# Performance work log

Hardware: AMD Instinct MI355X
Metric: run time of the kernel (lower is better)

Reference implementation:

```python
import jax, jax.numpy as jnp
import numpy as np

B, C, W, H = 8192, 512, 14, 4
D = C // H  # head dim = 128


def setup_inputs() -> dict:
    key = jax.random.key(0)
    ks = jax.random.split(key, 8)
    s = 1.0 / np.sqrt(C).astype(np.float32)
    return {
        "x": jax.random.normal(ks[0], (B, C, W), jnp.float32),
        "Wq": jax.random.normal(ks[1], (C, C), jnp.float32) * s,
        "bq": jax.random.normal(ks[2], (C,), jnp.float32) * 0.01,
        "Wk": jax.random.normal(ks[3], (C, C), jnp.float32) * s,
        "bk": jax.random.normal(ks[4], (C,), jnp.float32) * 0.01,
        "Wv": jax.random.normal(ks[5], (C, C), jnp.float32) * s,
        "bv": jax.random.normal(ks[6], (C,), jnp.float32) * 0.01,
        "rel_w": jax.random.normal(ks[7], (1, H, D, W), jnp.float32),
    }


def reference(x, Wq, bq, Wk, bk, Wv, bv, rel_w):
    # Conv1d(kernel_size=1) == channel-wise linear: out[b,o,w] = sum_c Wm[o,c]*x[b,c,w] + bm[o]
    def proj(Wm, bm):
        y = jnp.einsum('oc,bcw->bow', Wm, x) + bm[None, :, None]
        return y.reshape(B, H, D, W)

    q = proj(Wq, bq)  # [B,H,D,W]
    k = proj(Wk, bk)
    v = proj(Wv, bv)

    # content-content: q^T k over head dim -> [B,H,W,W]
    cc = jnp.einsum('bhdi,bhdj->bhij', q, k)
    # content-position: rel_w^T q -> [B,H,W,W] (rows = relative position, cols = query pos)
    cp = jnp.einsum('hdi,bhdj->bhij', rel_w[0], q)

    attn = jax.nn.softmax(cc + cp, axis=-1)  # softmax over last dim, as in the original

    # out = v @ attn^T : out[b,h,d,i] = sum_j v[b,h,d,j] * attn[b,h,i,j]
    out = jnp.einsum('bhdj,bhij->bhdi', v, attn)
    return out.reshape(B, C, W)
```

## Files before the change

### kernel.cpp

```cpp
#include <hip/hip_runtime.h>
#include <hip/hip_bf16.h>

typedef __bf16 bf16x8 __attribute__((ext_vector_type(8)));
typedef float f32x4 __attribute__((ext_vector_type(4)));
typedef int i32x4 __attribute__((ext_vector_type(4)));

typedef __attribute__((address_space(1))) const void GVoid;
typedef __attribute__((address_space(3))) void LVoid;

#define SX1 16.0f
#define SX1I 0.0625f
#define SX2 4000.0f
#define SW1 400.0f
#define SW1I 0.0025f
#define SW2 100000.0f
#define SR1 32.0f
#define SR1I 0.03125f
#define SR2 8000.0f
#define SC_QK 1.5625e-4f
#define SC_CP 1.953125e-3f
#define CORR 0.004f
#define QKS 4096.0f
#define QKSI 2.44140625e-4f
#define QKSI2 5.9604644775390625e-8f
#define CPS 256.0f
#define CPSI 3.90625e-3f

static __device__ __forceinline__ float b2f(unsigned short u) {
    union { float f; unsigned int i; } x; x.i = ((unsigned int)u) << 16; return x.f;
}
static __device__ __forceinline__ unsigned short f2b(float f) {
    union { float f; unsigned int u; } x; x.f = f;
    unsigned int r = x.u + 0x7FFFu + ((x.u >> 16) & 1u);
    return (unsigned short)(r >> 16);
}
static __device__ __forceinline__ int q8v(float v, float s) {
    int i = __float2int_rn(v * s);
    return (i > 127) ? 127 : (i < -127 ? -127 : i);
}
static __device__ __forceinline__ short f2s(float v, float s) {
    int i = __float2int_rn(v * s);
    i = (i > 32767) ? 32767 : (i < -32767 ? -32767 : i);
    return (short)i;
}
static __device__ __forceinline__ float s2f(unsigned int pair, int hi, float sc) {
    short s = hi ? (short)(pair >> 16) : (short)(pair & 0xffffu);
    return (float)s * sc;
}
static __device__ __forceinline__ void cvt8(uint4 r, float* o) {
    o[0] = (float)(short)(r.x & 0xffffu); o[1] = (float)(short)(r.x >> 16);
    o[2] = (float)(short)(r.y & 0xffffu); o[3] = (float)(short)(r.y >> 16);
    o[4] = (float)(short)(r.z & 0xffffu); o[5] = (float)(short)(r.z >> 16);
    o[6] = (float)(short)(r.w & 0xffffu); o[7] = (float)(short)(r.w >> 16);
}

__global__ __launch_bounds__(256) void k_prep(const float* __restrict__ Wq, const float* __restrict__ Wk,
                                              const float* __restrict__ Wv, const float* __restrict__ bq,
                                              const float* __restrict__ bk, const float* __restrict__ bv,
                                              const float* __restrict__ relw, char* __restrict__ Wi8,
                                              float* __restrict__ biasA) {
    int o = blockIdx.x;
    int tid = threadIdx.x;
    if (o < 1024) {
        const float* src = (o < 512) ? (Wq + (long)o * 512) : (Wk + (long)(o - 512) * 512);
        char* row = Wi8 + (long)o * 1024;
        for (int c = tid; c < 512; c += 256) {
            float w = src[c];
            int wh = q8v(w, SW1);
            float res = w - (float)wh * SW1I;
            int wl = q8v(res, SW2);
            row[c] = (char)wh;
            row[512 + c] = (char)wl;
        }
    } else if (o < 1536) {
        const float* src = Wv + (long)(o - 1024) * 512;
        char* row = Wi8 + (long)(1152 + (o - 1024)) * 1024;
        for (int c = tid; c < 512; c += 256) {
            float w = src[c];
            int wh = q8v(w, SW1);
            float res = w - (float)wh * SW1I;
            int wl = q8v(res, SW2);
            row[c] = (char)wh;
            row[512 + c] = (char)wl;
        }
    } else if (o < 1592) {
        int t = o - 1536, h = t / 14, i = t - h * 14;
        char* row = Wi8 + (long)(1024 + t) * 1024;
#pragma unroll
        for (int cc = 0; cc < 2; ++cc) {
            int c = tid + cc * 256;
            float acc = 0.f;
            for (int d = 0; d < 128; ++d)
                acc += relw[h * 1792 + d * 14 + i] * Wq[(long)(h * 128 + d) * 512 + c];
            int rh = q8v(acc, SR1);
            float res = acc - (float)rh * SR1I;
            int rl = q8v(res, SR2);
            row[c] = (char)rh;
            row[512 + c] = (char)rl;
        }
        if (tid == 0) {
            float acc = 0.f;
            for (int d = 0; d < 128; ++d) acc += relw[h * 1792 + d * 14 + i] * bq[h * 128 + d];
            biasA[1024 + t] = acc;
        }
    } else {
        for (int i = tid; i < 1664; i += 256) {
            if (i >= 1024 && i < 1080) continue;
            biasA[i] = (i < 512) ? bq[i] : (i < 1024) ? bk[i - 512] : (i < 1152) ? 0.f : bv[i - 1152];
        }
        int* z = (int*)(Wi8 + (long)1080 * 1024);
        for (int idx = tid; idx < 72 * 256; idx += 256) z[idx] = 0;
    }
}

__global__ __launch_bounds__(256) void k_transpose(const float* __restrict__ x,
                                                   char* __restrict__ Ai8, int b0) {
    __shared__ float xl[512 * 15];
    const float* xb = x + (long)(b0 + blockIdx.x) * 7168;
    const float4* xb4 = (const float4*)xb;
    int tid = threadIdx.x;
#pragma unroll
    for (int it = 0; it < 7; ++it) {
        int f = tid + it * 256;
        float4 v = xb4[f];
        float vals[4] = {v.x, v.y, v.z, v.w};
        int e = f * 4;
#pragma unroll
        for (int j = 0; j < 4; ++j) {
            int ee = e + j;
            int c = (ee * 9363) >> 17;
            int w = ee - c * 14;
            xl[c * 15 + w] = vals[j];
        }
    }
    __syncthreads();
    char* irow = Ai8 + (long)blockIdx.x * 14336;
#pragma unroll
    for (int it = 0; it < 7; ++it) {
        int p = tid + it * 256;
        int w = p >> 7, c0 = (p & 127) * 4;
        unsigned int hp = 0, lp = 0;
#pragma unroll
        for (int j = 0; j < 4; ++j) {
            float v = xl[(c0 + j) * 15 + w];
            int xh = q8v(v, SX1);
            float res = v - (float)xh * SX1I;
            int xlo = q8v(res, SX2);
            hp |= ((unsigned int)(xh & 255)) << (8 * j);
            lp |= ((unsigned int)(xlo & 255)) << (8 * j);
        }
        *(unsigned int*)(irow + (long)w * 1024 + c0) = hp;
        *(unsigned int*)(irow + (long)w * 1024 + 512 + c0) = lp;
    }
}

__global__ __launch_bounds__(256, 2) void k_gemmA(const char* __restrict__ Ai8,
                                                  const char* __restrict__ Wi8,
                                                  const float* __restrict__ biasA,
                                                  short* __restrict__ qkI,
                                                  unsigned short* __restrict__ vb, int Mtiles) {
    __shared__ __align__(16) char Ls[2][4][128 * 64];
    int nwg = Mtiles * 13;
    int p = blockIdx.x;
    int xcd = p & 7, o8 = p >> 3;
    int q8_ = nwg >> 3, r8 = nwg & 7;
    int t = (xcd < r8 ? xcd * (q8_ + 1) : r8 * (q8_ + 1) + (xcd - r8) * q8_) + o8;
    int mt = t / 13, nt = t - mt * 13;
    long m0 = (long)mt * 128;
    int n0 = nt * 128;
    bool isv = (nt >= 9);
    int tid = threadIdx.x, lane = tid & 63, wv = tid >> 6;
    int wr = wv >> 1, wc = wv & 1;

    i32x4 accM[4][4], accC[4][4];
#pragma unroll
    for (int i = 0; i < 4; ++i)
#pragma unroll
        for (int j = 0; j < 4; ++j) { accM[i][j] = (i32x4){0, 0, 0, 0}; accC[i][j] = (i32x4){0, 0, 0, 0}; }

#define STAGE(KT, BUF)                                                                           \
    {                                                                                            \
        int kof = (KT) * 64;                                                                     \
        _Pragma("unroll") for (int i = 0; i < 2; ++i) {                                          \
            int row = i * 64 + (tid >> 2);                                                       \
            int gu = (((tid & 3) + (row >> 1)) & 3) << 4;                                        \
            long ao = ((m0 + row) << 10) + kof + gu;                                             \
            long bo = ((long)(n0 + row) << 10) + kof + gu;                                       \
            int dof = i * 4096 + tid * 16;                                                       \
            __builtin_amdgcn_global_load_lds((GVoid*)(Ai8 + ao), (LVoid*)(&Ls[BUF][0][0] + dof), 16, 0, 0); \
            __builtin_amdgcn_global_load_lds((GVoid*)(Ai8 + ao + 512), (LVoid*)(&Ls[BUF][1][0] + dof), 16, 0, 0); \
            __builtin_amdgcn_global_load_lds((GVoid*)(Wi8 + bo), (LVoid*)(&Ls[BUF][2][0] + dof), 16, 0, 0); \
            __builtin_amdgcn_global_load_lds((GVoid*)(Wi8 + bo + 512), (LVoid*)(&Ls[BUF][3][0] + dof), 16, 0, 0); \
        }                                                                                        \
    }

    STAGE(0, 0);
    STAGE(1, 1);
    asm volatile("s_waitcnt vmcnt(8)" ::: "memory");
    __builtin_amdgcn_s_barrier();

    int cur = 0;
    for (int kt = 0; kt < 8; ++kt) {
        const char* Ah = &Ls[cur][0][0];
        const char* Al = &Ls[cur][1][0];
        const char* Bh = &Ls[cur][2][0];
        const char* Bl = &Ls[cur][3][0];
        int U = lane >> 4;
        i32x4 ah[4], al[4], bh[4], bl[4];
#pragma unroll
        for (int mf = 0; mf < 4; ++mf) {
            int row = wr * 64 + mf * 16 + (lane & 15);
            int off = row * 64 + (((U - (row >> 1)) & 3) << 4);
            ah[mf] = *(const i32x4*)(Ah + off);
            al[mf] = *(const i32x4*)(Al + off);
        }
#pragma unroll
        for (int nf = 0; nf < 4; ++nf) {
            int row = wc * 64 + nf * 16 + (lane & 15);
            int off = row * 64 + (((U - (row >> 1)) & 3) << 4);
            bh[nf] = *(const i32x4*)(Bh + off);
            bl[nf] = *(const i32x4*)(Bl + off);
        }
        asm volatile("s_waitcnt lgkmcnt(0)" ::: "memory");
        __builtin_amdgcn_sched_barrier(0);
        __builtin_amdgcn_s_barrier();
        if (kt + 2 < 8) STAGE(kt + 2, cur);

        __builtin_amdgcn_s_setprio(1);
#pragma unroll
        for (int mf = 0; mf < 4; ++mf)
#pragma unroll
            for (int nf = 0; nf < 4; ++nf)
                accM[mf][nf] = __builtin_amdgcn_mfma_i32_16x16x64_i8(ah[mf], bh[nf], accM[mf][nf], 0, 0, 0);
#pragma unroll
        for (int mf = 0; mf < 4; ++mf)
#pragma unroll
            for (int nf = 0; nf < 4; ++nf) {
                accC[mf][nf] = __builtin_amdgcn_mfma_i32_16x16x64_i8(al[mf], bh[nf], accC[mf][nf], 0, 0, 0);
                accC[mf][nf] = __builtin_amdgcn_mfma_i32_16x16x64_i8(ah[mf], bl[nf], accC[mf][nf], 0, 0, 0);
            }
        __builtin_amdgcn_s_setprio(0);

        if (kt < 6) asm volatile("s_waitcnt vmcnt(8)" ::: "memory");
        else        asm volatile("s_waitcnt vmcnt(0)" ::: "memory");
        __builtin_amdgcn_sched_barrier(0);
        __builtin_amdgcn_s_barrier();
        cur ^= 1;
    }
#undef STAGE

    unsigned short* eb = (unsigned short*)&Ls[0][0][0];
#pragma unroll
    for (int nf = 0; nf < 4; ++nf) {
        int ncol = wc * 64 + nf * 16 + (lane & 15);
        int n = n0 + ncol;
        float scale = (n < 1024) ? SC_QK : (n < 1152 ? SC_CP : SC_QK);
        float qsc = (n < 1024) ? QKS : CPS;
        float bb = biasA[n];
#pragma unroll
        for (int mf = 0; mf < 4; ++mf) {
            int rl0 = wr * 64 + mf * 16 + ((lane >> 4) << 2);
#pragma unroll
            for (int r = 0; r < 4; ++r) {
                float val = ((float)accM[mf][nf][r] + CORR * (float)accC[mf][nf][r]) * scale + bb;
                unsigned short sv = isv ? f2b(val) : (unsigned short)f2s(val, qsc);
                int row = rl0 + r;
                eb[row * 128 + ((((ncol >> 3) ^ (row & 7)) << 3) | (ncol & 7))] = sv;
            }
        }
    }
    __syncthreads();
    {
        int row = tid >> 1, half = tid & 1;
        long rb = isv ? ((m0 + row) * 1024 + (long)(n0 - 1152) * 2)
                      : ((m0 + row) * 2304 + (long)n0 * 2);
        char* dst = (isv ? (char*)vb : (char*)qkI) + rb + half * 128;
        const char* src = (const char*)eb + row * 256;
#pragma unroll
        for (int j = 0; j < 8; ++j) {
            int u = half * 8 + j;
            int up = u ^ (row & 7);
            *(uint4*)(dst + j * 16) = *(const uint4*)(src + up * 16);
        }
    }
}

__global__ __launch_bounds__(512) void k_attn(const short* __restrict__ qkI,
                                              const unsigned short* __restrict__ vb,
                                              float* __restrict__ out, int b0) {
    __shared__ unsigned short qsI[14 * 512];
    __shared__ unsigned short ksI[14 * 512];
    __shared__ float sl[56 * 16];
    int tid = threadIdx.x;
    long mb = (long)blockIdx.x * 14;
    const uint4* qk16 = (const uint4*)qkI;
#pragma unroll
    for (int it = 0; it < 4; ++it) {
        int idx = tid + it * 512;
        if (idx < 1792) {
            int w = idx >> 7, c8 = idx & 127;
            uint4 raw = qk16[(mb + w) * 144 + c8];
            int u = c8 & 63;
            unsigned short* base = (c8 < 64) ? qsI : ksI;
            *(uint4*)&base[w * 512 + ((u ^ (w & 7)) << 3)] = raw;
        }
    }
    __syncthreads();
    if (tid < 196) {
        int h = tid / 49, r = tid - h * 49;
        int i0 = (r / 7) * 2, j0 = (r - (r / 7) * 7) * 2;
        float a00 = 0.f, a01 = 0.f, a10 = 0.f, a11 = 0.f;
#pragma unroll
        for (int d8 = 0; d8 < 16; ++d8) {
            int uu = h * 16 + d8;
            uint4 ra = *(const uint4*)&qsI[i0 * 512 + ((uu ^ (i0 & 7)) << 3)];
            uint4 rb = *(const uint4*)&qsI[(i0 + 1) * 512 + ((uu ^ ((i0 + 1) & 7)) << 3)];
            uint4 rc = *(const uint4*)&ksI[j0 * 512 + ((uu ^ (j0 & 7)) << 3)];
            uint4 rd = *(const uint4*)&ksI[(j0 + 1) * 512 + ((uu ^ ((j0 + 1) & 7)) << 3)];
            float qa[8], qb[8], ka[8], kb[8];
            cvt8(ra, qa); cvt8(rb, qb); cvt8(rc, ka); cvt8(rd, kb);
#pragma unroll
            for (int e = 0; e < 8; ++e) {
                a00 += qa[e] * ka[e];
                a01 += qa[e] * kb[e];
                a10 += qb[e] * ka[e];
                a11 += qb[e] * kb[e];
            }
        }
        unsigned int cpa = *(const unsigned int*)&qkI[(mb + j0) * 1152 + 1024 + h * 14 + i0];
        unsigned int cpb = *(const unsigned int*)&qkI[(mb + j0 + 1) * 1152 + 1024 + h * 14 + i0];
        int base = (h * 14 + i0) * 16 + j0;
        sl[base]      = a00 * QKSI2 + s2f(cpa, 0, CPSI);
        sl[base + 16] = a10 * QKSI2 + s2f(cpa, 1, CPSI);
        sl[base + 1]  = a01 * QKSI2 + s2f(cpb, 0, CPSI);
        sl[base + 17] = a11 * QKSI2 + s2f(cpb, 1, CPSI);
    }
    __syncthreads();
    if (tid < 56) {
        float* row = &sl[tid * 16];
        float m = row[0];
#pragma unroll
        for (int j = 1; j < 14; ++j) m = fmaxf(m, row[j]);
        float ex[14]; float sum = 0.f;
#pragma unroll
        for (int j = 0; j < 14; ++j) { ex[j] = __expf(row[j] - m); sum += ex[j]; }
        float inv = 1.f / sum;
#pragma unroll
        for (int j = 0; j < 14; ++j) row[j] = ex[j] * inv;
    }
    __syncthreads();
    int c = tid, h = c >> 7;
    float vr[14];
#pragma unroll
    for (int j = 0; j < 14; ++j) vr[j] = b2f(vb[(mb + j) * 512 + c]);
    float* orow = out + (((long)(b0 + blockIdx.x) * 512 + c) * 14);
    float ob[14];
#pragma unroll
    for (int i = 0; i < 14; ++i) {
        const float* ar = &sl[(h * 14 + i) * 16];
        float a = 0.f;
#pragma unroll
        for (int j = 0; j < 14; ++j) a += vr[j] * ar[j];
        ob[i] = a;
    }
#pragma unroll
    for (int t2 = 0; t2 < 7; ++t2)
        *(float2*)(orow + t2 * 2) = make_float2(ob[2 * t2], ob[2 * t2 + 1]);
}

extern "C" void kernel_launch(void* const* d_in, const int* in_sizes, int n_in,
                              void* d_out, int out_size, void* d_ws, size_t ws_size,
                              hipStream_t stream) {
    const float* x    = (const float*)d_in[0];
    const float* Wq   = (const float*)d_in[1];
    const float* bq   = (const float*)d_in[2];
    const float* Wk   = (const float*)d_in[3];
    const float* bk   = (const float*)d_in[4];
    const float* Wv   = (const float*)d_in[5];
    const float* bv   = (const float*)d_in[6];
    const float* relw = (const float*)d_in[7];
    float* out = (float*)d_out;
    char* ws = (char*)d_ws;

    char*  Wi8   = ws;
    float* biasA = (float*)(ws + 1703936);
    const long WS_DATA = 1712128;

    long avail = (long)ws_size - WS_DATA;
    long nbmax = avail / 60928;
    long NBc = (nbmax / 128) * 128;
    if (NBc > 2048) NBc = 2048;
    if (NBc < 128) NBc = 128;

    char*           Ai8 = ws + WS_DATA;
    short*          qkI = (short*)(Ai8 + NBc * 14336);
    unsigned short* vbw = (unsigned short*)(qkI + NBc * 16128);

    k_prep<<<1593, 256, 0, stream>>>(Wq, Wk, Wv, bq, bk, bv, relw, Wi8, biasA);

    for (int b0 = 0; b0 < 8192; b0 += (int)NBc) {
        int nb = 8192 - b0; if (nb > NBc) nb = (int)NBc;
        int Mtiles = (nb * 14) / 128;
        k_transpose<<<nb, 256, 0, stream>>>(x, Ai8, b0);
        k_gemmA<<<Mtiles * 13, 256, 0, stream>>>(Ai8, Wi8, biasA, qkI, vbw, Mtiles);
        k_attn<<<nb, 512, 0, stream>>>(qkI, vbw, out, b0);
    }
}
```

Before: 636.7 us.

## Load GEMM operands directly from global memory into registers, dropping LDS staging

Replaces the double-buffered global_load_lds staging and its barriers in the int8 projection GEMM with direct per-lane 16-byte global loads into MFMA operand registers. The shared buffer shrinks to just the epilogue tile. This removes LDS round-trips and block-wide synchronisation, but operands are no longer shared across waves, so each wave re-reads A/B rows from global or L2. There is also no explicit prefetch overlap, leaving load latency exposed unless the compiler hides it.

```diff
diff --git a/kernel.cpp b/kernel.cpp
--- a/kernel.cpp
+++ b/kernel.cpp
@@ -159,7 +159,7 @@
                                                   const float* __restrict__ biasA,
                                                   short* __restrict__ qkI,
                                                   unsigned short* __restrict__ vb, int Mtiles) {
-    __shared__ __align__(16) char Ls[2][4][128 * 64];
+    __shared__ __align__(16) unsigned short eb[128 * 128];
     int nwg = Mtiles * 13;
     int p = blockIdx.x;
     int xcd = p & 7, o8 = p >> 3;
@@ -171,6 +171,17 @@
     bool isv = (nt >= 9);
     int tid = threadIdx.x, lane = tid & 63, wv = tid >> 6;
     int wr = wv >> 1, wc = wv & 1;
+    int U = lane >> 4;
+    int lr = lane & 15;
+
+    const char* Ab[4];
+    const char* Bb[4];
+#pragma unroll
+    for (int mf = 0; mf < 4; ++mf)
+        Ab[mf] = Ai8 + ((m0 + wr * 64 + mf * 16 + lr) << 10) + U * 16;
+#pragma unroll
+    for (int nf = 0; nf < 4; ++nf)
+        Bb[nf] = Wi8 + ((long)(n0 + wc * 64 + nf * 16 + lr) << 10) + U * 16;
 
     i32x4 accM[4][4], accC[4][4];
 #pragma unroll
@@ -178,53 +189,17 @@
 #pragma unroll
         for (int j = 0; j < 4; ++j) { accM[i][j] = (i32x4){0, 0, 0, 0}; accC[i][j] = (i32x4){0, 0, 0, 0}; }
 
-#define STAGE(KT, BUF)                                                                           \
-    {                                                                                            \
-        int kof = (KT) * 64;                                                                     \
-        _Pragma("unroll") for (int i = 0; i < 2; ++i) {                                          \
-            int row = i * 64 + (tid >> 2);                                                       \
-            int gu = (((tid & 3) + (row >> 1)) & 3) << 4;                                        \
-            long ao = ((m0 + row) << 10) + kof + gu;                                             \
-            long bo = ((long)(n0 + row) << 10) + kof + gu;                                       \
-            int dof = i * 4096 + tid * 16;                                                       \
-            __builtin_amdgcn_global_load_lds((GVoid*)(Ai8 + ao), (LVoid*)(&Ls[BUF][0][0] + dof), 16, 0, 0); \
-            __builtin_amdgcn_global_load_lds((GVoid*)(Ai8 + ao + 512), (LVoid*)(&Ls[BUF][1][0] + dof), 16, 0, 0); \
-            __builtin_amdgcn_global_load_lds((GVoid*)(Wi8 + bo), (LVoid*)(&Ls[BUF][2][0] + dof), 16, 0, 0); \
-            __builtin_amdgcn_global_load_lds((GVoid*)(Wi8 + bo + 512), (LVoid*)(&Ls[BUF][3][0] + dof), 16, 0, 0); \
-        }                                                                                        \
-    }
-
-    STAGE(0, 0);
-    STAGE(1, 1);
-    asm volatile("s_waitcnt vmcnt(8)" ::: "memory");
-    __builtin_amdgcn_s_barrier();
-
-    int cur = 0;
     for (int kt = 0; kt < 8; ++kt) {
-        const char* Ah = &Ls[cur][0][0];
-        const char* Al = &Ls[cur][1][0];
-        const char* Bh = &Ls[cur][2][0];
-        const char* Bl = &Ls[cur][3][0];
-        int U = lane >> 4;
-        i32x4 ah[4], al[4], bh[4], bl[4];
-#pragma unroll
-        for (int mf = 0; mf < 4; ++mf) {
-            int row = wr * 64 + mf * 16 + (lane & 15);
-            int off = row * 64 + (((U - (row >> 1)) & 3) << 4);
-            ah[mf] = *(const i32x4*)(Ah + off);
-            al[mf] = *(const i32x4*)(Al + off);
-        }
-#pragma unroll
-        for (int nf = 0; nf < 4; ++nf) {
-            int row = wc * 64 + nf * 16 + (lane & 15);
-            int off = row * 64 + (((U - (row >> 1)) & 3) << 4);
-            bh[nf] = *(const i32x4*)(Bh + off);
-            bl[nf] = *(const i32x4*)(Bl + off);
-        }
-        asm volatile("s_waitcnt lgkmcnt(0)" ::: "memory");
-        __builtin_amdgcn_sched_barrier(0);
-        __builtin_amdgcn_s_barrier();
-        if (kt + 2 < 8) STAGE(kt + 2, cur);
+        int kof = kt * 64;
+        i32x4 ah[4], bh[4], al[4], bl[4];
+#pragma unroll
+        for (int mf = 0; mf < 4; ++mf) ah[mf] = *(const i32x4*)(Ab[mf] + kof);
+#pragma unroll
+        for (int nf = 0; nf < 4; ++nf) bh[nf] = *(const i32x4*)(Bb[nf] + kof);
+#pragma unroll
+        for (int mf = 0; mf < 4; ++mf) al[mf] = *(const i32x4*)(Ab[mf] + kof + 512);
+#pragma unroll
+        for (int nf = 0; nf < 4; ++nf) bl[nf] = *(const i32x4*)(Bb[nf] + kof + 512);
 
         __builtin_amdgcn_s_setprio(1);
 #pragma unroll
@@ -240,16 +215,8 @@
                 accC[mf][nf] = __builtin_amdgcn_mfma_i32_16x16x64_i8(ah[mf], bl[nf], accC[mf][nf], 0, 0, 0);
             }
         __builtin_amdgcn_s_setprio(0);
-
-        if (kt < 6) asm volatile("s_waitcnt vmcnt(8)" ::: "memory");
-        else        asm volatile("s_waitcnt vmcnt(0)" ::: "memory");
-        __builtin_amdgcn_sched_barrier(0);
-        __builtin_amdgcn_s_barrier();
-        cur ^= 1;
-    }
-#undef STAGE
-
-    unsigned short* eb = (unsigned short*)&Ls[0][0][0];
+    }
+
 #pragma unroll
     for (int nf = 0; nf < 4; ++nf) {
         int ncol = wc * 64 + nf * 16 + (lane & 15);
```

After: 1.034 ms. +62.4%, slower.

## Enlarge int8 GEMM tile to 256 rows with 512-thread workgroups

Applied to the files above, without the earlier changes.

Doubles the M dimension of the k_gemmA output tile from 128 to 256 rows and uses 512 threads (8 waves) per workgroup. The weight tile in LDS is now shared by twice as many activation rows. The aim is to halve weight-tile global loads per output and cut the number of workgroups. LDS per block grows to 96KB, which likely limits occupancy to one block per CU. Barriers now synchronise 8 waves instead of 4.

```diff
diff --git a/kernel.cpp b/kernel.cpp
--- a/kernel.cpp
+++ b/kernel.cpp
@@ -154,19 +154,19 @@
     }
 }
 
-__global__ __launch_bounds__(256, 2) void k_gemmA(const char* __restrict__ Ai8,
+__global__ __launch_bounds__(512, 2) void k_gemmA(const char* __restrict__ Ai8,
                                                   const char* __restrict__ Wi8,
                                                   const float* __restrict__ biasA,
                                                   short* __restrict__ qkI,
                                                   unsigned short* __restrict__ vb, int Mtiles) {
-    __shared__ __align__(16) char Ls[2][4][128 * 64];
+    __shared__ __align__(16) char Ls[2][49152];
     int nwg = Mtiles * 13;
     int p = blockIdx.x;
     int xcd = p & 7, o8 = p >> 3;
     int q8_ = nwg >> 3, r8 = nwg & 7;
     int t = (xcd < r8 ? xcd * (q8_ + 1) : r8 * (q8_ + 1) + (xcd - r8) * q8_) + o8;
     int mt = t / 13, nt = t - mt * 13;
-    long m0 = (long)mt * 128;
+    long m0 = (long)mt * 256;
     int n0 = nt * 128;
     bool isv = (nt >= 9);
     int tid = threadIdx.x, lane = tid & 63, wv = tid >> 6;
@@ -182,29 +182,34 @@
     {                                                                                            \
         int kof = (KT) * 64;                                                                     \
         _Pragma("unroll") for (int i = 0; i < 2; ++i) {                                          \
-            int row = i * 64 + (tid >> 2);                                                       \
+            int row = i * 128 + (tid >> 2);                                                      \
             int gu = (((tid & 3) + (row >> 1)) & 3) << 4;                                        \
             long ao = ((m0 + row) << 10) + kof + gu;                                             \
-            long bo = ((long)(n0 + row) << 10) + kof + gu;                                       \
-            int dof = i * 4096 + tid * 16;                                                       \
-            __builtin_amdgcn_global_load_lds((GVoid*)(Ai8 + ao), (LVoid*)(&Ls[BUF][0][0] + dof), 16, 0, 0); \
-            __builtin_amdgcn_global_load_lds((GVoid*)(Ai8 + ao + 512), (LVoid*)(&Ls[BUF][1][0] + dof), 16, 0, 0); \
-            __builtin_amdgcn_global_load_lds((GVoid*)(Wi8 + bo), (LVoid*)(&Ls[BUF][2][0] + dof), 16, 0, 0); \
-            __builtin_amdgcn_global_load_lds((GVoid*)(Wi8 + bo + 512), (LVoid*)(&Ls[BUF][3][0] + dof), 16, 0, 0); \
+            int dof = i * 8192 + tid * 16;                                                       \
+            __builtin_amdgcn_global_load_lds((GVoid*)(Ai8 + ao), (LVoid*)(&Ls[BUF][0] + dof), 16, 0, 0);     \
+            __builtin_amdgcn_global_load_lds((GVoid*)(Ai8 + ao + 512), (LVoid*)(&Ls[BUF][16384] + dof), 16, 0, 0); \
+        }                                                                                        \
+        {                                                                                        \
+            int brow = tid >> 2;                                                                 \
+            int bgu = (((tid & 3) + (brow >> 1)) & 3) << 4;                                      \
+            long bo = ((long)(n0 + brow) << 10) + kof + bgu;                                     \
+            int bdof = tid * 16;                                                                 \
+            __builtin_amdgcn_global_load_lds((GVoid*)(Wi8 + bo), (LVoid*)(&Ls[BUF][32768] + bdof), 16, 0, 0);      \
+            __builtin_amdgcn_global_load_lds((GVoid*)(Wi8 + bo + 512), (LVoid*)(&Ls[BUF][40960] + bdof), 16, 0, 0); \
         }                                                                                        \
     }
 
     STAGE(0, 0);
     STAGE(1, 1);
-    asm volatile("s_waitcnt vmcnt(8)" ::: "memory");
+    asm volatile("s_waitcnt vmcnt(6)" ::: "memory");
     __builtin_amdgcn_s_barrier();
 
     int cur = 0;
     for (int kt = 0; kt < 8; ++kt) {
-        const char* Ah = &Ls[cur][0][0];
-        const char* Al = &Ls[cur][1][0];
-        const char* Bh = &Ls[cur][2][0];
-        const char* Bl = &Ls[cur][3][0];
+        const char* Ah = &Ls[cur][0];
+        const char* Al = &Ls[cur][16384];
+        const char* Bh = &Ls[cur][32768];
+        const char* Bl = &Ls[cur][40960];
         int U = lane >> 4;
         i32x4 ah[4], al[4], bh[4], bl[4];
 #pragma unroll
@@ -241,7 +246,7 @@
             }
         __builtin_amdgcn_s_setprio(0);
 
-        if (kt < 6) asm volatile("s_waitcnt vmcnt(8)" ::: "memory");
+        if (kt < 6) asm volatile("s_waitcnt vmcnt(6)" ::: "memory");
         else        asm volatile("s_waitcnt vmcnt(0)" ::: "memory");
         __builtin_amdgcn_sched_barrier(0);
         __builtin_amdgcn_s_barrier();
@@ -249,7 +254,7 @@
     }
 #undef STAGE
 
-    unsigned short* eb = (unsigned short*)&Ls[0][0][0];
+    unsigned short* eb = (unsigned short*)&Ls[0][0];
 #pragma unroll
     for (int nf = 0; nf < 4; ++nf) {
         int ncol = wc * 64 + nf * 16 + (lane & 15);
@@ -400,9 +405,9 @@
 
     for (int b0 = 0; b0 < 8192; b0 += (int)NBc) {
         int nb = 8192 - b0; if (nb > NBc) nb = (int)NBc;
-        int Mtiles = (nb * 14) / 128;
+        int M = nb * 14;
         k_transpose<<<nb, 256, 0, stream>>>(x, Ai8, b0);
-        k_gemmA<<<Mtiles * 13, 256, 0, stream>>>(Ai8, Wi8, biasA, qkI, vbw, Mtiles);
+        k_gemmA<<<(M / 256) * 13, 512, 0, stream>>>(Ai8, Wi8, biasA, qkI, vbw, M / 256);
         k_attn<<<nb, 512, 0, stream>>>(qkI, vbw, out, b0);
     }
 }
```

Result: slower. 732.8 us (+15.1%).

## Fuse GEMM and attention into one kernel, overlapping chunk N GEMM with chunk N-1 attention

Applied to the files above, without the earlier changes.

Merges the projection GEMM and attention kernels into a single launch. Each launch runs the GEMM blocks for the current batch chunk alongside the attention blocks for the previous chunk, with double-buffered q/k/v workspaces. The goal is to fill idle CUs during each phase's tail and cut one launch per chunk. In exchange it doubles the intermediate workspace, which can shrink the chunk size. Attention blocks drop to 256 threads, and every block of the combined kernel carries the larger 64KB shared allocation.

```diff
diff --git a/kernel.cpp b/kernel.cpp
--- a/kernel.cpp
+++ b/kernel.cpp
@@ -154,29 +154,36 @@
     }
 }
 
-__global__ __launch_bounds__(256, 2) void k_gemmA(const char* __restrict__ Ai8,
+__global__ __launch_bounds__(256, 2) void k_fused(const char* __restrict__ Ai8,
                                                   const char* __restrict__ Wi8,
                                                   const float* __restrict__ biasA,
-                                                  short* __restrict__ qkI,
-                                                  unsigned short* __restrict__ vb, int Mtiles) {
-    __shared__ __align__(16) char Ls[2][4][128 * 64];
-    int nwg = Mtiles * 13;
-    int p = blockIdx.x;
-    int xcd = p & 7, o8 = p >> 3;
-    int q8_ = nwg >> 3, r8 = nwg & 7;
-    int t = (xcd < r8 ? xcd * (q8_ + 1) : r8 * (q8_ + 1) + (xcd - r8) * q8_) + o8;
-    int mt = t / 13, nt = t - mt * 13;
-    long m0 = (long)mt * 128;
-    int n0 = nt * 128;
-    bool isv = (nt >= 9);
-    int tid = threadIdx.x, lane = tid & 63, wv = tid >> 6;
-    int wr = wv >> 1, wc = wv & 1;
-
-    i32x4 accM[4][4], accC[4][4];
-#pragma unroll
-    for (int i = 0; i < 4; ++i)
-#pragma unroll
-        for (int j = 0; j < 4; ++j) { accM[i][j] = (i32x4){0, 0, 0, 0}; accC[i][j] = (i32x4){0, 0, 0, 0}; }
+                                                  short* __restrict__ qkW,
+                                                  unsigned short* __restrict__ vbW, int Mtiles,
+                                                  const short* __restrict__ qkR,
+                                                  const unsigned short* __restrict__ vbR,
+                                                  float* __restrict__ out, int b0a) {
+    __shared__ __align__(16) char LS[65536];
+    int nG = Mtiles * 13;
+    int tid = threadIdx.x;
+
+    if ((int)blockIdx.x < nG) {
+        int nwg = nG;
+        int p = blockIdx.x;
+        int xcd = p & 7, o8 = p >> 3;
+        int q8_ = nwg >> 3, r8 = nwg & 7;
+        int t = (xcd < r8 ? xcd * (q8_ + 1) : r8 * (q8_ + 1) + (xcd - r8) * q8_) + o8;
+        int mt = t / 13, nt = t - mt * 13;
+        long m0 = (long)mt * 128;
+        int n0 = nt * 128;
+        bool isv = (nt >= 9);
+        int lane = tid & 63, wv = tid >> 6;
+        int wr = wv >> 1, wc = wv & 1;
+
+        i32x4 accM[4][4], accC[4][4];
+#pragma unroll
+        for (int i = 0; i < 4; ++i)
+#pragma unroll
+            for (int j = 0; j < 4; ++j) { accM[i][j] = (i32x4){0, 0, 0, 0}; accC[i][j] = (i32x4){0, 0, 0, 0}; }
 
 #define STAGE(KT, BUF)                                                                           \
     {                                                                                            \
@@ -186,186 +193,184 @@
             int gu = (((tid & 3) + (row >> 1)) & 3) << 4;                                        \
             long ao = ((m0 + row) << 10) + kof + gu;                                             \
             long bo = ((long)(n0 + row) << 10) + kof + gu;                                       \
-            int dof = i * 4096 + tid * 16;                                                       \
-            __builtin_amdgcn_global_load_lds((GVoid*)(Ai8 + ao), (LVoid*)(&Ls[BUF][0][0] + dof), 16, 0, 0); \
-            __builtin_amdgcn_global_load_lds((GVoid*)(Ai8 + ao + 512), (LVoid*)(&Ls[BUF][1][0] + dof), 16, 0, 0); \
-            __builtin_amdgcn_global_load_lds((GVoid*)(Wi8 + bo), (LVoid*)(&Ls[BUF][2][0] + dof), 16, 0, 0); \
-            __builtin_amdgcn_global_load_lds((GVoid*)(Wi8 + bo + 512), (LVoid*)(&Ls[BUF][3][0] + dof), 16, 0, 0); \
+            int dof = (BUF) * 32768 + i * 4096 + tid * 16;                                       \
+            __builtin_amdgcn_global_load_lds((GVoid*)(Ai8 + ao), (LVoid*)(LS + dof), 16, 0, 0);          \
+            __builtin_amdgcn_global_load_lds((GVoid*)(Ai8 + ao + 512), (LVoid*)(LS + 8192 + dof), 16, 0, 0);  \
+            __builtin_amdgcn_global_load_lds((GVoid*)(Wi8 + bo), (LVoid*)(LS + 16384 + dof), 16, 0, 0);       \
+            __builtin_amdgcn_global_load_lds((GVoid*)(Wi8 + bo + 512), (LVoid*)(LS + 24576 + dof), 16, 0, 0); \
         }                                                                                        \
     }
 
-    STAGE(0, 0);
-    STAGE(1, 1);
-    asm volatile("s_waitcnt vmcnt(8)" ::: "memory");
-    __builtin_amdgcn_s_barrier();
-
-    int cur = 0;
-    for (int kt = 0; kt < 8; ++kt) {
-        const char* Ah = &Ls[cur][0][0];
-        const char* Al = &Ls[cur][1][0];
-        const char* Bh = &Ls[cur][2][0];
-        const char* Bl = &Ls[cur][3][0];
-        int U = lane >> 4;
-        i32x4 ah[4], al[4], bh[4], bl[4];
-#pragma unroll
-        for (int mf = 0; mf < 4; ++mf) {
-            int row = wr * 64 + mf * 16 + (lane & 15);
-            int off = row * 64 + (((U - (row >> 1)) & 3) << 4);
-            ah[mf] = *(const i32x4*)(Ah + off);
-            al[mf] = *(const i32x4*)(Al + off);
-        }
+        STAGE(0, 0);
+        STAGE(1, 1);
+        asm volatile("s_waitcnt vmcnt(8)" ::: "memory");
+        __builtin_amdgcn_s_barrier();
+
+        int cur = 0;
+        for (int kt = 0; kt < 8; ++kt) {
+            const char* Ah = LS + cur * 32768;
+            const char* Al = Ah + 8192;
+            const char* Bh = Ah + 16384;
+            const char* Bl = Ah + 24576;
+            int U = lane >> 4;
+            i32x4 ah[4], al[4], bh[4], bl[4];
+#pragma unroll
+            for (int mf = 0; mf < 4; ++mf) {
+                int row = wr * 64 + mf * 16 + (lane & 15);
+                int off = row * 64 + (((U - (row >> 1)) & 3) << 4);
+                ah[mf] = *(const i32x4*)(Ah + off);
+                al[mf] = *(const i32x4*)(Al + off);
+            }
+#pragma unroll
+            for (int nf = 0; nf < 4; ++nf) {
+                int row = wc * 64 + nf * 16 + (lane & 15);
+                int off = row * 64 + (((U - (row >> 1)) & 3) << 4);
+                bh[nf] = *(const i32x4*)(Bh + off);
+                bl[nf] = *(const i32x4*)(Bl + off);
+            }
+            asm volatile("s_waitcnt lgkmcnt(0)" ::: "memory");
+            __builtin_amdgcn_sched_barrier(0);
+            __builtin_amdgcn_s_barrier();
+            if (kt + 2 < 8) STAGE(kt + 2, cur);
+
+            __builtin_amdgcn_s_setprio(1);
+#pragma unroll
+            for (int mf = 0; mf < 4; ++mf)
+#pragma unroll
+                for (int nf = 0; nf < 4; ++nf)
+                    accM[mf][nf] = __builtin_amdgcn_mfma_i32_16x16x64_i8(ah[mf], bh[nf], accM[mf][nf], 0, 0, 0);
+#pragma unroll
+            for (int mf = 0; mf < 4; ++mf)
+#pragma unroll
+                for (int nf = 0; nf < 4; ++nf) {
+                    accC[mf][nf] = __builtin_amdgcn_mfma_i32_16x16x64_i8(al[mf], bh[nf], accC[mf][nf], 0, 0, 0);
+                    accC[mf][nf] = __builtin_amdgcn_mfma_i32_16x16x64_i8(ah[mf], bl[nf], accC[mf][nf], 0, 0, 0);
+                }
+            __builtin_amdgcn_s_setprio(0);
+
+            if (kt < 6) asm volatile("s_waitcnt vmcnt(8)" ::: "memory");
+            else        asm volatile("s_waitcnt vmcnt(0)" ::: "memory");
+            __builtin_amdgcn_sched_barrier(0);
+            __builtin_amdgcn_s_barrier();
+            cur ^= 1;
+        }
+#undef STAGE
+
+        unsigned short* eb = (unsigned short*)LS;
 #pragma unroll
         for (int nf = 0; nf < 4; ++nf) {
-            int row = wc * 64 + nf * 16 + (lane & 15);
-            int off = row * 64 + (((U - (row >> 1)) & 3) << 4);
-            bh[nf] = *(const i32x4*)(Bh + off);
-            bl[nf] = *(const i32x4*)(Bl + off);
-        }
-        asm volatile("s_waitcnt lgkmcnt(0)" ::: "memory");
-        __builtin_amdgcn_sched_barrier(0);
-        __builtin_amdgcn_s_barrier();
-        if (kt + 2 < 8) STAGE(kt + 2, cur);
-
-        __builtin_amdgcn_s_setprio(1);
-#pragma unroll
-        for (int mf = 0; mf < 4; ++mf)
-#pragma unroll
-            for (int nf = 0; nf < 4; ++nf)
-                accM[mf][nf] = __builtin_amdgcn_mfma_i32_16x16x64_i8(ah[mf], bh[nf], accM[mf][nf], 0, 0, 0);
-#pragma unroll
-        for (int mf = 0; mf < 4; ++mf)
-#pragma unroll
-            for (int nf = 0; nf < 4; ++nf) {
-                accC[mf][nf] = __builtin_amdgcn_mfma_i32_16x16x64_i8(al[mf], bh[nf], accC[mf][nf], 0, 0, 0);
-                accC[mf][nf] = __builtin_amdgcn_mfma_i32_16x16x64_i8(ah[mf], bl[nf], accC[mf][nf], 0, 0, 0);
-            }
-        __builtin_amdgcn_s_setprio(0);
-
-        if (kt < 6) asm volatile("s_waitcnt vmcnt(8)" ::: "memory");
-        else        asm volatile("s_waitcnt vmcnt(0)" ::: "memory");
-        __builtin_amdgcn_sched_barrier(0);
-        __builtin_amdgcn_s_barrier();
-        cur ^= 1;
-    }
-#undef STAGE
-
-    unsigned short* eb = (unsigned short*)&Ls[0][0][0];
-#pragma unroll
-    for (int nf = 0; nf < 4; ++nf) {
-        int ncol = wc * 64 + nf * 16 + (lane & 15);
-        int n = n0 + ncol;
-        float scale = (n < 1024) ? SC_QK : (n < 1152 ? SC_CP : SC_QK);
-        float qsc = (n < 1024) ? QKS : CPS;
-        float bb = biasA[n];
-#pragma unroll
-        for (int mf = 0; mf < 4; ++mf) {
-            int rl0 = wr * 64 + mf * 16 + ((lane >> 4) << 2);
-#pragma unroll
-            for (int r = 0; r < 4; ++r) {
-                float val = ((float)accM[mf][nf][r] + CORR * (float)accC[mf][nf][r]) * scale + bb;
-                unsigned short sv = isv ? f2b(val) : (unsigned short)f2s(val, qsc);
-                int row = rl0 + r;
-                eb[row * 128 + ((((ncol >> 3) ^ (row & 7)) << 3) | (ncol & 7))] = sv;
-            }
-        }
-    }
-    __syncthreads();
-    {
-        int row = tid >> 1, half = tid & 1;
-        long rb = isv ? ((m0 + row) * 1024 + (long)(n0 - 1152) * 2)
-                      : ((m0 + row) * 2304 + (long)n0 * 2);
-        char* dst = (isv ? (char*)vb : (char*)qkI) + rb + half * 128;
-        const char* src = (const char*)eb + row * 256;
-#pragma unroll
-        for (int j = 0; j < 8; ++j) {
-            int u = half * 8 + j;
-            int up = u ^ (row & 7);
-            *(uint4*)(dst + j * 16) = *(const uint4*)(src + up * 16);
-        }
-    }
-}
-
-__global__ __launch_bounds__(512) void k_attn(const short* __restrict__ qkI,
-                                              const unsigned short* __restrict__ vb,
-                                              float* __restrict__ out, int b0) {
-    __shared__ unsigned short qsI[14 * 512];
-    __shared__ unsigned short ksI[14 * 512];
-    __shared__ float sl[56 * 16];
-    int tid = threadIdx.x;
-    long mb = (long)blockIdx.x * 14;
-    const uint4* qk16 = (const uint4*)qkI;
-#pragma unroll
-    for (int it = 0; it < 4; ++it) {
-        int idx = tid + it * 512;
-        if (idx < 1792) {
+            int ncol = wc * 64 + nf * 16 + (lane & 15);
+            int n = n0 + ncol;
+            float scale = (n < 1024) ? SC_QK : (n < 1152 ? SC_CP : SC_QK);
+            float qsc = (n < 1024) ? QKS : CPS;
+            float bb = biasA[n];
+#pragma unroll
+            for (int mf = 0; mf < 4; ++mf) {
+                int rl0 = wr * 64 + mf * 16 + ((lane >> 4) << 2);
+#pragma unroll
+                for (int r = 0; r < 4; ++r) {
+                    float val = ((float)accM[mf][nf][r] + CORR * (float)accC[mf][nf][r]) * scale + bb;
+                    unsigned short sv = isv ? f2b(val) : (unsigned short)f2s(val, qsc);
+                    int row = rl0 + r;
+                    eb[row * 128 + ((((ncol >> 3) ^ (row & 7)) << 3) | (ncol & 7))] = sv;
+                }
+            }
+        }
+        __syncthreads();
+        {
+            int row = tid >> 1, half = tid & 1;
+            long rb = isv ? ((m0 + row) * 1024 + (long)(n0 - 1152) * 2)
+                          : ((m0 + row) * 2304 + (long)n0 * 2);
+            char* dst = (isv ? (char*)vbW : (char*)qkW) + rb + half * 128;
+            const char* src = (const char*)eb + row * 256;
+#pragma unroll
+            for (int j = 0; j < 8; ++j) {
+                int u = half * 8 + j;
+                int up = u ^ (row & 7);
+                *(uint4*)(dst + j * 16) = *(const uint4*)(src + up * 16);
+            }
+        }
+    } else {
+        unsigned short* qsI = (unsigned short*)LS;
+        unsigned short* ksI = (unsigned short*)(LS + 14336);
+        float* sl = (float*)(LS + 28672);
+        int ab = (int)blockIdx.x - nG;
+        long mb = (long)ab * 14;
+        const uint4* qk16 = (const uint4*)qkR;
+#pragma unroll
+        for (int it = 0; it < 7; ++it) {
+            int idx = tid + it * 256;
             int w = idx >> 7, c8 = idx & 127;
             uint4 raw = qk16[(mb + w) * 144 + c8];
             int u = c8 & 63;
             unsigned short* base = (c8 < 64) ? qsI : ksI;
             *(uint4*)&base[w * 512 + ((u ^ (w & 7)) << 3)] = raw;
         }
-    }
-    __syncthreads();
-    if (tid < 196) {
-        int h = tid / 49, r = tid - h * 49;
-        int i0 = (r / 7) * 2, j0 = (r - (r / 7) * 7) * 2;
-        float a00 = 0.f, a01 = 0.f, a10 = 0.f, a11 = 0.f;
-#pragma unroll
-        for (int d8 = 0; d8 < 16; ++d8) {
-            int uu = h * 16 + d8;
-            uint4 ra = *(const uint4*)&qsI[i0 * 512 + ((uu ^ (i0 & 7)) << 3)];
-            uint4 rb = *(const uint4*)&qsI[(i0 + 1) * 512 + ((uu ^ ((i0 + 1) & 7)) << 3)];
-            uint4 rc = *(const uint4*)&ksI[j0 * 512 + ((uu ^ (j0 & 7)) << 3)];
-            uint4 rd = *(const uint4*)&ksI[(j0 + 1) * 512 + ((uu ^ ((j0 + 1) & 7)) << 3)];
-            float qa[8], qb[8], ka[8], kb[8];
-            cvt8(ra, qa); cvt8(rb, qb); cvt8(rc, ka); cvt8(rd, kb);
-#pragma unroll
-            for (int e = 0; e < 8; ++e) {
-                a00 += qa[e] * ka[e];
-                a01 += qa[e] * kb[e];
-                a10 += qb[e] * ka[e];
-                a11 += qb[e] * kb[e];
-            }
-        }
-        unsigned int cpa = *(const unsigned int*)&qkI[(mb + j0) * 1152 + 1024 + h * 14 + i0];
-        unsigned int cpb = *(const unsigned int*)&qkI[(mb + j0 + 1) * 1152 + 1024 + h * 14 + i0];
-        int base = (h * 14 + i0) * 16 + j0;
-        sl[base]      = a00 * QKSI2 + s2f(cpa, 0, CPSI);
-        sl[base + 16] = a10 * QKSI2 + s2f(cpa, 1, CPSI);
-        sl[base + 1]  = a01 * QKSI2 + s2f(cpb, 0, CPSI);
-        sl[base + 17] = a11 * QKSI2 + s2f(cpb, 1, CPSI);
-    }
-    __syncthreads();
-    if (tid < 56) {
-        float* row = &sl[tid * 16];
-        float m = row[0];
-#pragma unroll
-        for (int j = 1; j < 14; ++j) m = fmaxf(m, row[j]);
-        float ex[14]; float sum = 0.f;
-#pragma unroll
-        for (int j = 0; j < 14; ++j) { ex[j] = __expf(row[j] - m); sum += ex[j]; }
-        float inv = 1.f / sum;
-#pragma unroll
-        for (int j = 0; j < 14; ++j) row[j] = ex[j] * inv;
-    }
-    __syncthreads();
-    int c = tid, h = c >> 7;
-    float vr[14];
-#pragma unroll
-    for (int j = 0; j < 14; ++j) vr[j] = b2f(vb[(mb + j) * 512 + c]);
-    float* orow = out + (((long)(b0 + blockIdx.x) * 512 + c) * 14);
-    float ob[14];
-#pragma unroll
-    for (int i = 0; i < 14; ++i) {
-        const float* ar = &sl[(h * 14 + i) * 16];
-        float a = 0.f;
-#pragma unroll
-        for (int j = 0; j < 14; ++j) a += vr[j] * ar[j];
-        ob[i] = a;
-    }
-#pragma unroll
-    for (int t2 = 0; t2 < 7; ++t2)
-        *(float2*)(orow + t2 * 2) = make_float2(ob[2 * t2], ob[2 * t2 + 1]);
+        __syncthreads();
+        if (tid < 196) {
+            int h = tid / 49, r = tid - h * 49;
+            int i0 = (r / 7) * 2, j0 = (r - (r / 7) * 7) * 2;
+            float a00 = 0.f, a01 = 0.f, a10 = 0.f, a11 = 0.f;
+#pragma unroll
+            for (int d8 = 0; d8 < 16; ++d8) {
+                int uu = h * 16 + d8;
+                uint4 ra = *(const uint4*)&qsI[i0 * 512 + ((uu ^ (i0 & 7)) << 3)];
+                uint4 rb = *(const uint4*)&qsI[(i0 + 1) * 512 + ((uu ^ ((i0 + 1) & 7)) << 3)];
+                uint4 rc = *(const uint4*)&ksI[j0 * 512 + ((uu ^ (j0 & 7)) << 3)];
+                uint4 rd = *(const uint4*)&ksI[(j0 + 1) * 512 + ((uu ^ ((j0 + 1) & 7)) << 3)];
+                float qa[8], qb[8], ka[8], kb[8];
+                cvt8(ra, qa); cvt8(rb, qb); cvt8(rc, ka); cvt8(rd, kb);
+#pragma unroll
+                for (int e = 0; e < 8; ++e) {
+                    a00 += qa[e] * ka[e];
+                    a01 += qa[e] * kb[e];
+                    a10 += qb[e] * ka[e];
+                    a11 += qb[e] * kb[e];
+                }
+            }
+            unsigned int cpa = *(const unsigned int*)&qkR[(mb + j0) * 1152 + 1024 + h * 14 + i0];
+            unsigned int cpb = *(const unsigned int*)&qkR[(mb + j0 + 1) * 1152 + 1024 + h * 14 + i0];
+            int base = (h * 14 + i0) * 16 + j0;
+            sl[base]      = a00 * QKSI2 + s2f(cpa, 0, CPSI);
+            sl[base + 16] = a10 * QKSI2 + s2f(cpa, 1, CPSI);
+            sl[base + 1]  = a01 * QKSI2 + s2f(cpb, 0, CPSI);
+            sl[base + 17] = a11 * QKSI2 + s2f(cpb, 1, CPSI);
+        }
+        __syncthreads();
+        if (tid < 56) {
+            float* row = &sl[tid * 16];
+            float m = row[0];
+#pragma unroll
+            for (int j = 1; j < 14; ++j) m = fmaxf(m, row[j]);
+            float ex[14]; float sum = 0.f;
+#pragma unroll
+            for (int j = 0; j < 14; ++j) { ex[j] = __expf(row[j] - m); sum += ex[j]; }
+            float inv = 1.f / sum;
+#pragma unroll
+            for (int j = 0; j < 14; ++j) row[j] = ex[j] * inv;
+        }
+        __syncthreads();
+#pragma unroll
+        for (int cc = 0; cc < 2; ++cc) {
+            int c = tid + cc * 256, h = c >> 7;
+            float vr[14];
+#pragma unroll
+            for (int j = 0; j < 14; ++j) vr[j] = b2f(vbR[(mb + j) * 512 + c]);
+            float* orow = out + (((long)(b0a + ab) * 512 + c) * 14);
+            float ob[14];
+#pragma unroll
+            for (int i = 0; i < 14; ++i) {
+                const float* ar = &sl[(h * 14 + i) * 16];
+                float a = 0.f;
+#pragma unroll
+                for (int j = 0; j < 14; ++j) a += vr[j] * ar[j];
+                ob[i] = a;
+            }
+#pragma unroll
+            for (int t2 = 0; t2 < 7; ++t2)
+                *(float2*)(orow + t2 * 2) = make_float2(ob[2 * t2], ob[2 * t2 + 1]);
+        }
+    }
 }
 
 extern "C" void kernel_launch(void* const* d_in, const int* in_sizes, int n_in,
@@ -387,22 +392,37 @@
     const long WS_DATA = 1712128;
 
     long avail = (long)ws_size - WS_DATA;
-    long nbmax = avail / 60928;
+    long nbmax = avail / 107520;
     long NBc = (nbmax / 128) * 128;
     if (NBc > 2048) NBc = 2048;
     if (NBc < 128) NBc = 128;
 
-    char*           Ai8 = ws + WS_DATA;
-    short*          qkI = (short*)(Ai8 + NBc * 14336);
-    unsigned short* vbw = (unsigned short*)(qkI + NBc * 16128);
+    char*           Ai8  = ws + WS_DATA;
+    short*          qkI0 = (short*)(Ai8 + NBc * 14336);
+    short*          qkI1 = qkI0 + NBc * 16128;
+    unsigned short* vb0  = (unsigned short*)(qkI1 + NBc * 16128);
+    unsigned short* vb1  = vb0 + NBc * 7168;
 
     k_prep<<<1593, 256, 0, stream>>>(Wq, Wk, Wv, bq, bk, bv, relw, Wi8, biasA);
 
+    int par = 0, prev_par = 0, prev_nb = 0, prev_b0 = 0;
     for (int b0 = 0; b0 < 8192; b0 += (int)NBc) {
         int nb = 8192 - b0; if (nb > NBc) nb = (int)NBc;
+        k_transpose<<<nb, 256, 0, stream>>>(x, Ai8, b0);
         int Mtiles = (nb * 14) / 128;
-        k_transpose<<<nb, 256, 0, stream>>>(x, Ai8, b0);
-        k_gemmA<<<Mtiles * 13, 256, 0, stream>>>(Ai8, Wi8, biasA, qkI, vbw, Mtiles);
-        k_attn<<<nb, 512, 0, stream>>>(qkI, vbw, out, b0);
-    }
-}
+        int nG = Mtiles * 13;
+        short* qw = par ? qkI1 : qkI0;
+        unsigned short* vw = par ? vb1 : vb0;
+        const short* qr = prev_par ? qkI1 : qkI0;
+        const unsigned short* vr = prev_par ? vb1 : vb0;
+        k_fused<<<nG + prev_nb, 256, 0, stream>>>(Ai8, Wi8, biasA, qw, vw, Mtiles,
+                                                  qr, vr, out, prev_b0);
+        prev_nb = nb; prev_b0 = b0; prev_par = par; par ^= 1;
+    }
+    {
+        const short* qr = prev_par ? qkI1 : qkI0;
+        const unsigned short* vr = prev_par ? vb1 : vb0;
+        k_fused<<<prev_nb, 256, 0, stream>>>(Ai8, Wi8, biasA, nullptr, nullptr, 0,
+                                             qr, vr, out, prev_b0);
+    }
+}
```

Result: no change. 635.0 us (-0.3%).
